# Kernel optimization log

Hardware: AMD Instinct MI355X
Metric: run time of the kernel (lower is better)

The kernel has to match this reference:

```python
import jax, jax.numpy as jnp
import numpy as np
from jax.scipy.special import logsumexp

EPSILON = 0.01        # temperature
DIST_THRESH = 0.2
NUM_ITERS = 3
NEG_INF = -1.0e9

B, N, M, C = 4, 4096, 4096, 256


def setup_inputs() -> dict:
    key = jax.random.key(0)
    k1, k2, k3, k4, k5 = jax.random.split(key, 5)
    source_feats = jax.random.normal(k1, (B, N, C), dtype=jnp.float32)
    source_locs = jax.random.uniform(k2, (B, N, 2), dtype=jnp.float32)
    target_locs = jax.random.uniform(k3, (B, M, 2), dtype=jnp.float32)
    source_valid_mask = jax.random.bernoulli(k4, 0.9, (B, N))
    target_valid_mask = jax.random.bernoulli(k5, 0.9, (B, M))
    return {
        "source_feats": source_feats,
        "source_locs": source_locs,
        "target_locs": target_locs,
        "source_valid_mask": source_valid_mask,
        "target_valid_mask": target_valid_mask,
    }


def reference(source_feats, source_locs, target_locs, source_valid_mask, target_valid_mask):
    # pairwise squared distances: [B, M, N]
    diff = target_locs[:, :, None, :] - source_locs[:, None, :, :]  # [B, M, N, 2]
    dist_sq = jnp.sum(diff * diff, axis=-1)                          # [B, M, N]
    log_K = -dist_sq / (EPSILON + 1e-8)

    valid_connection = dist_sq < (DIST_THRESH ** 2)
    valid_connection = valid_connection & source_valid_mask[:, None, :]
    valid_connection = valid_connection & target_valid_mask[:, :, None]
    log_K = jnp.where(valid_connection, log_K, NEG_INF)

    # Sinkhorn iterations in log space
    v = jnp.zeros((log_K.shape[0], 1, log_K.shape[2]), dtype=log_K.dtype)  # [B,1,N]
    u = jnp.zeros((log_K.shape[0], log_K.shape[1], 1), dtype=log_K.dtype)  # [B,M,1]
    for _ in range(NUM_ITERS):
        u = -logsumexp(log_K + v, axis=2, keepdims=True)
        v = -logsumexp(log_K + u, axis=1, keepdims=True)
        v = jnp.where(source_valid_mask[:, None, :], v, 0.0)

    attn = jnp.exp(log_K + u + v)  # [B, M, N]
    attn = jax.lax.stop_gradient(attn)  # original computes it under torch.no_grad

    target_feats = jnp.einsum('bmn,bnc->bmc', attn, source_feats)
    target_feats = target_feats * target_valid_mask[:, :, None].astype(target_feats.dtype)
    has_source = jnp.any(valid_connection, axis=-1, keepdims=True)
    target_feats = target_feats * has_source.astype(target_feats.dtype)
    return target_feats
```

## Files before the change

kernel.cpp:

```cpp
#include <hip/hip_runtime.h>
#include <math.h>

#define BB 4
#define BN 4096
#define CC 256
constexpr float T2      = 0.04f;
constexpr float INV_EPS = (float)(1.0 / 0.01000001);

typedef __attribute__((ext_vector_type(8)))  short bf16x8;
typedef __attribute__((ext_vector_type(16))) float f32x16;

__device__ __forceinline__ int cell_of(float x, float y) {
  int cx = (int)(x * 5.0f); cx = cx < 0 ? 0 : (cx > 4 ? 4 : cx);
  int cy = (int)(y * 5.0f); cy = cy < 0 ? 0 : (cy > 4 ? 4 : cy);
  return cy * 5 + cx;
}

__device__ __forceinline__ void dma16(const void* g, void* l) {
  __builtin_amdgcn_global_load_lds(
      (const __attribute__((address_space(1))) void*)g,
      (__attribute__((address_space(3))) void*)l, 16, 0, 0);
}

__global__ __launch_bounds__(256) void k_bin(
    const float* __restrict__ tlocs, const float* __restrict__ slocs,
    const int* __restrict__ tmask, const int* __restrict__ smask,
    int* __restrict__ Zc,
    int* __restrict__ starts_t, int* __restrict__ starts_s,
    int* __restrict__ perm_t, int* __restrict__ perm_s,
    float4* __restrict__ t_sorted, float4* __restrict__ s_sorted) {
  const int which = blockIdx.x & 1, b = blockIdx.x >> 1;
  const float* locs = which ? slocs : tlocs;
  const int*   mask = which ? smask : tmask;
  int* starts       = which ? starts_s : starts_t;
  int* perm         = which ? perm_s : perm_t;
  float4* pack      = which ? s_sorted : t_sorted;
  const int tid = threadIdx.x;
  if (blockIdx.x == 0) Zc[tid] = 0;
  __shared__ int cnt[25];
  __shared__ int st[26];
  __shared__ int cur[25];
  if (tid < 25) cnt[tid] = 0;
  __syncthreads();
  for (int i = tid; i < BN; i += 256)
    atomicAdd(&cnt[cell_of(locs[(b * BN + i) * 2], locs[(b * BN + i) * 2 + 1])], 1);
  __syncthreads();
  if (tid == 0) {
    int acc = 0;
    for (int c = 0; c < 25; c++) { st[c] = acc; acc += cnt[c]; }
    st[25] = acc;
  }
  __syncthreads();
  if (tid < 25) cur[tid] = st[tid];
  if (tid < 26) starts[b * 32 + tid] = st[tid];
  __syncthreads();
  for (int i = tid; i < BN; i += 256) {
    float x = locs[(b * BN + i) * 2], y = locs[(b * BN + i) * 2 + 1];
    int pos = atomicAdd(&cur[cell_of(x, y)], 1);
    perm[b * BN + pos] = i;
    pack[b * BN + pos] = make_float4(x, y, 0.f, mask[b * BN + i] ? 1.f : 0.f);
  }
}

__global__ __launch_bounds__(256) void k_pack(
    const float* __restrict__ feats, const int* __restrict__ perm_s,
    unsigned* __restrict__ fB) {
  const int b   = blockIdx.x >> 8;
  const int blk = blockIdx.x & 255;
  const int tid = threadIdx.x;
  __shared__ float fs[16][260];
  __shared__ int   sidx[16];
  if (tid < 16) sidx[tid] = perm_s[b * BN + blk * 16 + tid];
  __syncthreads();
  #pragma unroll
  for (int q = 0; q < 4; q++) {
    int idx = q * 256 + tid;
    int r = idx >> 6, c4 = idx & 63;
    float4 v = ((const float4*)feats)[(((b << 12) + sidx[r]) << 6) + c4];
    fs[r][c4 * 4 + 0] = v.x; fs[r][c4 * 4 + 1] = v.y;
    fs[r][c4 * 4 + 2] = v.z; fs[r][c4 * 4 + 3] = v.w;
  }
  __syncthreads();
  const int ch = tid;
  unsigned* dst = fB + ((((size_t)b << 8) + blk) << 12) + ch * 16;
  unsigned pk[16];
  #pragma unroll
  for (int sl = 0; sl < 16; sl++) {
    float f = fs[sl][ch];
    unsigned fb = __float_as_uint(f);
    unsigned hb = fb & 0xFFFF0000u;
    float lo = f - __uint_as_float(hb);
    pk[sl ^ (((ch >> 1) & 3) << 2)] = hb | (__float_as_uint(lo) >> 16);
  }
  #pragma unroll
  for (int q = 0; q < 4; q++)
    ((uint4*)dst)[q] = make_uint4(pk[q*4], pk[q*4+1], pk[q*4+2], pk[q*4+3]);
}

__global__ __launch_bounds__(256) void k_sink(const float4* __restrict__ opp,
                                              float4* __restrict__ own,
                                              const int* __restrict__ opp_starts,
                                              const int* __restrict__ Zin,
                                              int* __restrict__ Zout,
                                              int zero_invalid) {
  const int wv   = threadIdx.x >> 6;
  const int lane = threadIdx.x & 63;
  const int rowb = blockIdx.x * 16 + wv * 4;
  const int b    = rowb >> 12;
  float4 me[4];
  float  s[4] = {0.f, 0.f, 0.f, 0.f};
  int ryLo = 5, ryHi = -1, rxLo = 5, rxHi = -1;
  #pragma unroll
  for (int i = 0; i < 4; i++) {
    me[i] = own[rowb + i];
    if (me[i].w != 0.f) {
      int cell = cell_of(me[i].x, me[i].y);
      int cy = cell / 5, cx = cell % 5;
      ryLo = min(ryLo, max(cy - 1, 0)); ryHi = max(ryHi, min(cy + 1, 4));
      rxLo = min(rxLo, max(cx - 1, 0)); rxHi = max(rxHi, min(cx + 1, 4));
    }
  }
  for (int ry = ryLo; ry <= ryHi; ry++) {
    const int r0 = opp_starts[b * 32 + ry * 5 + rxLo];
    const int r1 = opp_starts[b * 32 + ry * 5 + rxHi + 1];
    for (int j = r0 + lane; j < r1; j += 64) {
      float4 o = opp[b * BN + j];
      #pragma unroll
      for (int i = 0; i < 4; i++) {
        float dx = me[i].x - o.x, dy = me[i].y - o.y;
        float d2 = fmaf(dx, dx, dy * dy);
        bool  c  = (d2 < T2) && (o.w != 0.f) && (me[i].w != 0.f);
        float t  = c ? fmaf(d2, -INV_EPS, o.z) : -3e30f;
        s[i] += __expf(t);
      }
    }
  }
  #pragma unroll
  for (int i = 0; i < 4; i++)
    for (int off = 32; off > 0; off >>= 1) s[i] += __shfl_xor(s[i], off);
  if (lane == 0) {
    const float Zf = (float)Zin[b];
    #pragma unroll
    for (int i = 0; i < 4; i++) {
      float ss  = s[i] + Zf;
      float val = (ss > 0.f) ? -logf(ss) : 1.0e9f;
      if (zero_invalid && me[i].w == 0.f) val = 0.f;
      own[rowb + i] = make_float4(me[i].x, me[i].y, val, me[i].w);
      if (val == 1.0e9f) atomicAdd(&Zout[b], 1);
    }
  }
}

#define MAXCH 12

__global__ __launch_bounds__(256) void k_out(
    const unsigned* __restrict__ fB, const float4* __restrict__ t_sorted,
    const float4* __restrict__ s_sorted, const int* __restrict__ perm_t,
    const int* __restrict__ starts_t, const int* __restrict__ starts_s,
    float* __restrict__ out) {
  const int b = blockIdx.z;
  const int cell = blockIdx.y / 3, rsel = blockIdx.y % 3;
  const int cy = cell / 5, cx = cell % 5;
  const int ry = cy + rsel - 1;
  if (ry < 0 || ry > 4) return;
  const int t0 = starts_t[b * 32 + cell], t1 = starts_t[b * 32 + cell + 1];
  const int base = t0 + blockIdx.x * 32;
  if (base >= t1) return;
  const int rx0 = max(cx - 1, 0), rx1 = min(cx + 1, 4);
  const int s0 = starts_s[b * 32 + ry * 5 + rx0];
  const int s1 = starts_s[b * 32 + ry * 5 + rx1 + 1];
  if (s0 >= s1) return;
  const int nt = min(32, t1 - base);

  __shared__ __align__(16) unsigned pool[8576];
  __shared__ float4 tL[32];
  __shared__ int    morg[32];

  const int tid  = threadIdx.x;
  const int lane = tid & 63;
  const int w    = tid >> 6;

  if (tid < 32) {
    if (tid < nt) {
      tL[tid]   = t_sorted[b * BN + base + tid];
      morg[tid] = perm_t[b * BN + base + tid];
    } else {
      tL[tid]   = make_float4(0.f, 0.f, 0.f, 0.f);
      morg[tid] = 0;
    }
  }
  __syncthreads();

  const int kg = lane >> 5;
  const int ln = lane & 31;
  const float4 t4a = tL[ln];
  const int sB = b * BN;

  const int blk0 = s0 >> 4;
  const int nBlk = ((s1 + 15) >> 4) - blk0;

  {
    const unsigned* g = fB + ((((size_t)b << 8) + blk0) << 12);
    #pragma unroll
    for (int q = 0; q < 4; q++)
      dma16(g + (w * 4 + q) * 256 + lane * 4,
            (void*)(pool + (w * 4 + q) * 256));
  }
  float4 ps[8], pn[8];
  {
    int j0 = blk0 * 16 + kg * 8;
    #pragma unroll
    for (int e = 0; e < 8; e++)
      ps[e] = s_sorted[sB + min(j0 + e, BN - 1)];
  }

  f32x16 acc0, acc1;
  #pragma unroll
  for (int i = 0; i < 16; i++) { acc0[i] = 0.f; acc1[i] = 0.f; }

  int buf = 0;
  for (int r = 0; r < nBlk; r++, buf ^= 1) {
    asm volatile("s_waitcnt vmcnt(0)" ::: "memory");
    __builtin_amdgcn_s_barrier();
    __builtin_amdgcn_sched_barrier(0);
    const bool more = (r + 1 < nBlk);
    if (more) {
      const unsigned* g = fB + ((((size_t)b << 8) + blk0 + r + 1) << 12);
      #pragma unroll
      for (int q = 0; q < 4; q++)
        dma16(g + (w * 4 + q) * 256 + lane * 4,
              (void*)(pool + (buf ^ 1) * 4096 + (w * 4 + q) * 256));
      int j0n = (blk0 + r + 1) * 16 + kg * 8;
      #pragma unroll
      for (int e = 0; e < 8; e++)
        pn[e] = s_sorted[sB + min(j0n + e, BN - 1)];
    }
    const int j0 = (blk0 + r) * 16 + kg * 8;
    unsigned ahv[8], alv[8];
    #pragma unroll
    for (int e = 0; e < 8; e++) {
      float4 s4 = ps[e];
      int j = j0 + e;
      float dx = t4a.x - s4.x, dy = t4a.y - s4.y;
      float d2 = fmaf(dx, dx, dy * dy);
      bool  c  = (j >= s0) && (j < s1) && (d2 < T2) &&
                 (s4.w != 0.f) && (t4a.w != 0.f);
      float a  = c ? __expf(fmaf(d2, -INV_EPS, t4a.z + s4.z)) : 0.f;
      unsigned ab = __float_as_uint(a);
      unsigned hb = ab & 0xFFFF0000u;
      float alo = a - __uint_as_float(hb);
      ahv[e] = ab >> 16;
      alv[e] = __float_as_uint(alo) >> 16;
    }
    union { unsigned u[4]; bf16x8 v; } BH, BL;
    #pragma unroll
    for (int i = 0; i < 4; i++) {
      BH.u[i] = ahv[2*i] | (ahv[2*i+1] << 16);
      BL.u[i] = alv[2*i] | (alv[2*i+1] << 16);
    }
    const unsigned* tile = pool + buf * 4096;
    #pragma unroll
    for (int mt = 0; mt < 2; mt++) {
      const int chl = w * 64 + mt * 32 + ln;
      const int xv  = (chl >> 1) & 3;
      const int g0  = ((kg << 1) | 0) ^ xv;
      const int g1  = ((kg << 1) | 1) ^ xv;
      union { uint4 q[2]; unsigned u[8]; } A;
      A.q[0] = *(const uint4*)(tile + chl * 16 + g0 * 4);
      A.q[1] = *(const uint4*)(tile + chl * 16 + g1 * 4);
      union { unsigned u[4]; bf16x8 v; } AH, AL;
      #pragma unroll
      for (int i = 0; i < 4; i++) {
        AH.u[i] = (A.u[2*i] >> 16)     | (A.u[2*i+1] & 0xFFFF0000u);
        AL.u[i] = (A.u[2*i] & 0xFFFFu) | (A.u[2*i+1] << 16);
      }
      if (mt == 0) {
        acc0 = __builtin_amdgcn_mfma_f32_32x32x16_bf16(AH.v, BH.v, acc0, 0, 0, 0);
        acc0 = __builtin_amdgcn_mfma_f32_32x32x16_bf16(AH.v, BL.v, acc0, 0, 0, 0);
        acc0 = __builtin_amdgcn_mfma_f32_32x32x16_bf16(AL.v, BH.v, acc0, 0, 0, 0);
      } else {
        acc1 = __builtin_amdgcn_mfma_f32_32x32x16_bf16(AH.v, BH.v, acc1, 0, 0, 0);
        acc1 = __builtin_amdgcn_mfma_f32_32x32x16_bf16(AH.v, BL.v, acc1, 0, 0, 0);
        acc1 = __builtin_amdgcn_mfma_f32_32x32x16_bf16(AL.v, BH.v, acc1, 0, 0, 0);
      }
    }
    #pragma unroll
    for (int e = 0; e < 8; e++) ps[e] = pn[e];
  }

  __syncthreads();
  float* Dl = (float*)pool;
  #pragma unroll
  for (int mt = 0; mt < 2; mt++) {
    #pragma unroll
    for (int rg = 0; rg < 4; rg++) {
      int chb = w * 64 + mt * 32 + 8 * rg + 4 * kg;
      float4 v;
      if (mt == 0) v = make_float4(acc0[rg*4], acc0[rg*4+1], acc0[rg*4+2], acc0[rg*4+3]);
      else         v = make_float4(acc1[rg*4], acc1[rg*4+1], acc1[rg*4+2], acc1[rg*4+3]);
      *(float4*)&Dl[ln * 268 + chb] = v;
    }
  }
  __syncthreads();
  {
    const int tmg = tid >> 5, chg = tid & 31;
    #pragma unroll
    for (int i = 0; i < 4; i++) {
      int tm = tmg * 4 + i;
      if (tm < nt) {
        float* op = out + (((b << 12) + morg[tm]) << 8) + chg * 4;
        float4 d0 = *(float4*)&Dl[tm * 268 + chg * 4];
        float4 d1 = *(float4*)&Dl[tm * 268 + 128 + chg * 4];
        atomicAdd(op + 0, d0.x); atomicAdd(op + 1, d0.y);
        atomicAdd(op + 2, d0.z); atomicAdd(op + 3, d0.w);
        atomicAdd(op + 128, d1.x); atomicAdd(op + 129, d1.y);
        atomicAdd(op + 130, d1.z); atomicAdd(op + 131, d1.w);
      }
    }
  }
}

extern "C" void kernel_launch(void* const* d_in, const int* in_sizes, int n_in,
                              void* d_out, int out_size, void* d_ws, size_t ws_size,
                              hipStream_t stream) {
  const float* feats = (const float*)d_in[0];
  const float* slocs = (const float*)d_in[1];
  const float* tlocs = (const float*)d_in[2];
  const int*   smask = (const int*)d_in[3];
  const int*   tmask = (const int*)d_in[4];
  float* out = (float*)d_out;

  char* ws = (char*)d_ws;
  int*    Zc       = (int*)(ws + 1024);
  int*    starts_t = (int*)(ws + 2048);
  int*    starts_s = (int*)(ws + 2560);
  int*    perm_t   = (int*)(ws + 4096);
  int*    perm_s   = (int*)(ws + 69632);
  float4* s_sorted = (float4*)(ws + 135168);
  float4* t_sorted = (float4*)(ws + 397312);
  unsigned* fB     = (unsigned*)(ws + 663552);

  hipMemsetAsync(out, 0, (size_t)out_size * sizeof(float), stream);
  k_bin<<<8, 256, 0, stream>>>(tlocs, slocs, tmask, smask, Zc,
                               starts_t, starts_s, perm_t, perm_s,
                               t_sorted, s_sorted);
  k_pack<<<1024, 256, 0, stream>>>(feats, perm_s, fB);
  for (int it = 0; it < 3; it++) {
    k_sink<<<1024, 256, 0, stream>>>(s_sorted, t_sorted, starts_s,
                                     Zc + (it == 0 ? 0 : (2 * it) * 4),
                                     Zc + (2 * it + 1) * 4, 0);
    k_sink<<<1024, 256, 0, stream>>>(t_sorted, s_sorted, starts_t,
                                     Zc + (2 * it + 1) * 4,
                                     Zc + (2 * it + 2) * 4, 1);
  }
  k_out<<<dim3(MAXCH, 75, BB), 256, 0, stream>>>(fB, t_sorted, s_sorted,
                                                 perm_t, starts_t, starts_s,
                                                 out);
}
```

Before: 557.6 us.

## Triple-buffer feature tiles and DMA source locations into LDS

Replaces the double-buffered feature DMA with a three-deep ring so each tile is prefetched two iterations ahead, and waits with vmcnt(5) so only the oldest tile must have landed. Source location/potential records now also arrive by direct global-to-LDS DMA alongside each tile rather than through per-thread register loads. The goal is to hide global memory latency behind the MFMA work. In exchange, shared memory per block grows, which may lower occupancy, and redundant tail loads are issued when the ring runs past the last block.

```diff
diff --git a/kernel.cpp b/kernel.cpp
--- a/kernel.cpp
+++ b/kernel.cpp
@@ -20,6 +20,11 @@
   __builtin_amdgcn_global_load_lds(
       (const __attribute__((address_space(1))) void*)g,
       (__attribute__((address_space(3))) void*)l, 16, 0, 0);
+}
+__device__ __forceinline__ void dma4(const void* g, void* l) {
+  __builtin_amdgcn_global_load_lds(
+      (const __attribute__((address_space(1))) void*)g,
+      (__attribute__((address_space(3))) void*)l, 4, 0, 0);
 }
 
 __global__ __launch_bounds__(256) void k_bin(
@@ -152,6 +157,7 @@
 }
 
 #define MAXCH 12
+#define BUFU  4160
 
 __global__ __launch_bounds__(256) void k_out(
     const unsigned* __restrict__ fB, const float4* __restrict__ t_sorted,
@@ -172,7 +178,7 @@
   if (s0 >= s1) return;
   const int nt = min(32, t1 - base);
 
-  __shared__ __align__(16) unsigned pool[8576];
+  __shared__ __align__(16) unsigned pool[3 * BUFU];
   __shared__ float4 tL[32];
   __shared__ int    morg[32];
 
@@ -199,47 +205,36 @@
   const int blk0 = s0 >> 4;
   const int nBlk = ((s1 + 15) >> 4) - blk0;
 
-  {
-    const unsigned* g = fB + ((((size_t)b << 8) + blk0) << 12);
+  const unsigned* fBb = fB + (((size_t)b) << 20);
+  auto ISSUE = [&](int t, int bufI) {
+    const unsigned* g = fBb + ((size_t)t << 12);
+    unsigned* lb = pool + bufI * BUFU;
     #pragma unroll
     for (int q = 0; q < 4; q++)
-      dma16(g + (w * 4 + q) * 256 + lane * 4,
-            (void*)(pool + (w * 4 + q) * 256));
-  }
-  float4 ps[8], pn[8];
-  {
-    int j0 = blk0 * 16 + kg * 8;
-    #pragma unroll
-    for (int e = 0; e < 8; e++)
-      ps[e] = s_sorted[sB + min(j0 + e, BN - 1)];
-  }
+      dma16(g + (w * 4 + q) * 256 + lane * 4, (void*)(lb + (w * 4 + q) * 256));
+    dma4((const char*)s_sorted + ((size_t)(sB + t * 16) << 4) + lane * 4,
+         (void*)(lb + 4096));
+  };
+
+  ISSUE(blk0, 0);
+  ISSUE(blk0 + min(1, nBlk - 1), 1);
 
   f32x16 acc0, acc1;
   #pragma unroll
   for (int i = 0; i < 16; i++) { acc0[i] = 0.f; acc1[i] = 0.f; }
 
-  int buf = 0;
-  for (int r = 0; r < nBlk; r++, buf ^= 1) {
-    asm volatile("s_waitcnt vmcnt(0)" ::: "memory");
+  int cur = 0;
+  for (int r = 0; r < nBlk; r++) {
+    asm volatile("s_waitcnt vmcnt(5)" ::: "memory");
     __builtin_amdgcn_s_barrier();
     __builtin_amdgcn_sched_barrier(0);
-    const bool more = (r + 1 < nBlk);
-    if (more) {
-      const unsigned* g = fB + ((((size_t)b << 8) + blk0 + r + 1) << 12);
-      #pragma unroll
-      for (int q = 0; q < 4; q++)
-        dma16(g + (w * 4 + q) * 256 + lane * 4,
-              (void*)(pool + (buf ^ 1) * 4096 + (w * 4 + q) * 256));
-      int j0n = (blk0 + r + 1) * 16 + kg * 8;
-      #pragma unroll
-      for (int e = 0; e < 8; e++)
-        pn[e] = s_sorted[sB + min(j0n + e, BN - 1)];
-    }
+    ISSUE(blk0 + min(r + 2, nBlk - 1), cur == 0 ? 2 : cur - 1);
+    const unsigned* tile = pool + cur * BUFU;
     const int j0 = (blk0 + r) * 16 + kg * 8;
     unsigned ahv[8], alv[8];
     #pragma unroll
     for (int e = 0; e < 8; e++) {
-      float4 s4 = ps[e];
+      float4 s4 = *(const float4*)(tile + 4096 + (kg * 8 + e) * 4);
       int j = j0 + e;
       float dx = t4a.x - s4.x, dy = t4a.y - s4.y;
       float d2 = fmaf(dx, dx, dy * dy);
@@ -258,7 +253,6 @@
       BH.u[i] = ahv[2*i] | (ahv[2*i+1] << 16);
       BL.u[i] = alv[2*i] | (alv[2*i+1] << 16);
     }
-    const unsigned* tile = pool + buf * 4096;
     #pragma unroll
     for (int mt = 0; mt < 2; mt++) {
       const int chl = w * 64 + mt * 32 + ln;
@@ -284,10 +278,10 @@
         acc1 = __builtin_amdgcn_mfma_f32_32x32x16_bf16(AL.v, BH.v, acc1, 0, 0, 0);
       }
     }
-    #pragma unroll
-    for (int e = 0; e < 8; e++) ps[e] = pn[e];
-  }
-
+    cur = (cur == 2) ? 0 : cur + 1;
+  }
+
+  asm volatile("s_waitcnt vmcnt(0)" ::: "memory");
   __syncthreads();
   float* Dl = (float*)pool;
   #pragma unroll
```

After: 560.7 us. Within noise of the previous version (+0.5%).
